# Kernel tuning notes

Measured on AMD Instinct MI355X. Metric: run time of the kernel, lower is better.

The kernel has to match this reference:

```python
import jax, jax.numpy as jnp
import numpy as np

B, C_IN, H, W = 1, 3, 96, 96
NB_CLASSES = 21
NB_ITER = 5
THETA_ALPHA, THETA_BETA, THETA_GAMMA = 160.0, 3.0, 3.0


def setup_inputs() -> dict:
    key = jax.random.key(0)
    ks = jax.random.split(key, 8)
    image = jax.random.uniform(ks[0], (B, C_IN, H, W), jnp.float32)
    net_w = jax.random.normal(ks[1], (NB_CLASSES, C_IN, 3, 3), jnp.float32) * 0.1
    net_b = jax.random.normal(ks[2], (NB_CLASSES,), jnp.float32) * 0.01
    sp_w = jax.random.normal(ks[3], (NB_CLASSES, NB_CLASSES), jnp.float32) * 0.1
    sp_b = jnp.zeros((NB_CLASSES,), jnp.float32)
    bl_w = jax.random.normal(ks[4], (NB_CLASSES, NB_CLASSES), jnp.float32) * 0.1
    bl_b = jnp.zeros((NB_CLASSES,), jnp.float32)
    comp_w = jax.random.normal(ks[5], (NB_CLASSES, NB_CLASSES), jnp.float32) * 0.1
    comp_b = jnp.zeros((NB_CLASSES,), jnp.float32)
    return {"image": image, "net_w": net_w, "net_b": net_b,
            "sp_w": sp_w, "sp_b": sp_b, "bl_w": bl_w, "bl_b": bl_b,
            "comp_w": comp_w, "comp_b": comp_b}


def _gauss_kernel(feat):
    # feat: [B, N, D] -> K[B, N, N] = exp(-||f_i - f_j||^2 / 2)
    sq = jnp.sum(feat * feat, axis=-1)
    d2 = sq[:, :, None] + sq[:, None, :] - 2.0 * jnp.einsum('bnd,bmd->bnm', feat, feat)
    return jnp.exp(-0.5 * jnp.maximum(d2, 0.0))


def _crf_forward(image, net_w, net_b, sp_w, sp_b, bl_w, bl_b, comp_w, comp_b):
    b, c_in, h, w = image.shape
    n = h * w
    nb_classes = net_w.shape[0]
    # unary network: 3x3 same conv
    unaries = jax.lax.conv_general_dilated(
        image, net_w, (1, 1), 'SAME',
        dimension_numbers=('NCHW', 'OIHW', 'NCHW')) + net_b[None, :, None, None]
    # feature-space Gaussian kernels (exact form the permutohedral lattice approximates)
    yy, xx = jnp.meshgrid(jnp.arange(h, dtype=jnp.float32),
                          jnp.arange(w, dtype=jnp.float32), indexing='ij')
    pos = jnp.stack([xx.ravel(), yy.ravel()], axis=-1)          # [N, 2]
    pos_b = jnp.broadcast_to(pos, (b, n, 2))
    img_flat = image.reshape(b, c_in, n).transpose(0, 2, 1)      # [B, N, Cin]
    k_sp = _gauss_kernel(pos_b / THETA_GAMMA)                    # spatial kernel
    k_bl = _gauss_kernel(jnp.concatenate(
        [pos_b / THETA_ALPHA, img_flat / THETA_BETA], axis=-1))  # bilateral kernel
    norm_sp = k_sp.sum(-1)                                       # [B, N]
    norm_bl = k_bl.sum(-1)

    def filt(k, norm, s):
        return jnp.einsum('bnm,bcm->bcn', k, s) / norm[:, None, :]

    u = unaries.reshape(b, nb_classes, n)
    q = u
    s = jax.nn.softmax(q, axis=1)
    for _ in range(NB_ITER):
        sp = filt(k_sp, norm_sp, s)
        bl = filt(k_bl, norm_bl, s)
        mp = (jnp.einsum('oc,bcn->bon', sp_w, sp) + sp_b[None, :, None]
              + jnp.einsum('oc,bcn->bon', bl_w, bl) + bl_b[None, :, None])
        pairwise = jnp.einsum('oc,bcn->bon', comp_w, mp) + comp_b[None, :, None]
        q = u - pairwise
        s = jax.nn.softmax(q, axis=1)
    return s.reshape(b, nb_classes, h, w)


def reference(image, net_w, net_b, sp_w, sp_b, bl_w, bl_b, comp_w, comp_b):
    return _crf_forward(image, net_w, net_b, sp_w, sp_b, bl_w, bl_b, comp_w, comp_b)
```

## Files before the change

### kernel.cpp

```cpp
#include <hip/hip_runtime.h>

#define NPIX 9216
#define IMH 96
#define IMW 96
#define NC 21
#define NCH 22
#define CP 24
#define NMON 126
#define RAD 15
#define NITER 5
#define MG 11
#define NMG 12
#define LDSS 260
#define MPAD 2816

__constant__ float GW[16] = {
    1.0f, 0.945959f, 0.800737f, 0.606531f, 0.411112f, 0.249352f,
    0.135335f, 0.0657285f, 0.0285655f, 0.0111090f, 0.00386592f,
    0.00120386f, 0.000335463f, 8.36523e-05f, 1.86640e-05f, 3.72665e-06f};

__constant__ float d_bk[5] = {1.000000f, 0.998959f, 0.509936f, 0.139441f, 0.070024f};

__global__ __launch_bounds__(64) void prep_kernel(
    const float* __restrict__ img, const float* __restrict__ net_w,
    const float* __restrict__ net_b,
    float* __restrict__ u_pm, float* __restrict__ s_pm, float* __restrict__ s_cm,
    float* __restrict__ phi, float* __restrict__ M0)
{
    __shared__ float wsh[567], bsh[21];
    __shared__ float sg_sh[NMON];
    const int tid = threadIdx.x;
    for (int i = tid; i < 567; i += 64) wsh[i] = net_w[i];
    if (tid < 21) bsh[tid] = net_b[tid];
    for (int m = tid; m < NMON; m += 64) {
        int e1 = 0, e2 = 0, e3 = 0, e4 = 0, e5 = 0, cnt = 0;
        bool done = false;
        for (int a = 0; a <= 4 && !done; a++)
            for (int b2 = 0; b2 <= 4 - a && !done; b2++)
                for (int c = 0; c <= 4 - a - b2 && !done; c++)
                    for (int d = 0; d <= 4 - a - b2 - c && !done; d++) {
                        const int rem = 4 - a - b2 - c - d;
                        if (m - cnt <= rem) {
                            e1 = a; e2 = b2; e3 = c; e4 = d; e5 = m - cnt; done = true;
                        } else cnt += rem + 1;
                    }
        const float fact[5] = {1.f, 1.f, 2.f, 6.f, 24.f};
        const int k = e1 + e2 + e3 + e4 + e5;
        sg_sh[m] = sqrtf(d_bk[k] * fact[k] /
                         (fact[e1] * fact[e2] * fact[e3] * fact[e4] * fact[e5]));
    }
    __syncthreads();

    const int px = blockIdx.x * 64 + tid;
    const int i = px / IMW, j = px % IMW;
    if (px < 2772) M0[px] = 0.f;

    float acc[NC];
    #pragma unroll
    for (int o = 0; o < NC; o++) acc[o] = bsh[o];
    for (int ci = 0; ci < 3; ci++)
        for (int ky = 0; ky < 3; ky++)
            for (int kx = 0; kx < 3; kx++) {
                const int ii = i + ky - 1, jj = j + kx - 1;
                float v = 0.f;
                if (ii >= 0 && ii < IMH && jj >= 0 && jj < IMW)
                    v = img[(ci * IMH + ii) * IMW + jj];
                #pragma unroll
                for (int o = 0; o < NC; o++)
                    acc[o] = fmaf(v, wsh[(ci * 3 + ky) * 3 + kx + o * 27], acc[o]);
            }
    {
        float4* up = (float4*)(u_pm + (size_t)px * CP);
        up[0] = make_float4(acc[0], acc[1], acc[2], acc[3]);
        up[1] = make_float4(acc[4], acc[5], acc[6], acc[7]);
        up[2] = make_float4(acc[8], acc[9], acc[10], acc[11]);
        up[3] = make_float4(acc[12], acc[13], acc[14], acc[15]);
        up[4] = make_float4(acc[16], acc[17], acc[18], acc[19]);
        up[5] = make_float4(acc[20], 0.f, 0.f, 0.f);
    }
    float mx = acc[0];
    #pragma unroll
    for (int o = 1; o < NC; o++) mx = fmaxf(mx, acc[o]);
    float sum = 0.f;
    #pragma unroll
    for (int o = 0; o < NC; o++) { acc[o] = __expf(acc[o] - mx); sum += acc[o]; }
    const float inv = 1.f / sum;
    #pragma unroll
    for (int o = 0; o < NC; o++) acc[o] *= inv;
    {
        float4* sp = (float4*)(s_pm + (size_t)px * CP);
        sp[0] = make_float4(acc[0], acc[1], acc[2], acc[3]);
        sp[1] = make_float4(acc[4], acc[5], acc[6], acc[7]);
        sp[2] = make_float4(acc[8], acc[9], acc[10], acc[11]);
        sp[3] = make_float4(acc[12], acc[13], acc[14], acc[15]);
        sp[4] = make_float4(acc[16], acc[17], acc[18], acc[19]);
        sp[5] = make_float4(acc[20], 1.f, 0.f, 0.f);
    }
    #pragma unroll
    for (int o = 0; o < NC; o++) s_cm[(size_t)o * NPIX + px] = acc[o];
    s_cm[(size_t)21 * NPIX + px] = 1.f;

    const float fv[5] = {(float)j * (1.0f / 160.0f), (float)i * (1.0f / 160.0f),
                         img[0 * NPIX + px] * (1.0f / 3.0f),
                         img[1 * NPIX + px] * (1.0f / 3.0f),
                         img[2 * NPIX + px] * (1.0f / 3.0f)};
    const float env = __expf(-0.5f * (fv[0]*fv[0] + fv[1]*fv[1] + fv[2]*fv[2] +
                                      fv[3]*fv[3] + fv[4]*fv[4]));
    {
        int m = 0;
        float p1 = env;
        #pragma unroll
        for (int e1 = 0; e1 <= 4; e1++) {
            float p2 = p1;
            #pragma unroll
            for (int e2 = 0; e2 <= 4 - e1; e2++) {
                float p3 = p2;
                #pragma unroll
                for (int e3 = 0; e3 <= 4 - e1 - e2; e3++) {
                    float p4 = p3;
                    #pragma unroll
                    for (int e4 = 0; e4 <= 4 - e1 - e2 - e3; e4++) {
                        float p5 = p4;
                        #pragma unroll
                        for (int e5 = 0; e5 <= 4 - e1 - e2 - e3 - e4; e5++) {
                            phi[(size_t)m * NPIX + px] = sg_sh[m] * p5;
                            ++m;
                            p5 *= fv[4];
                        }
                        p4 *= fv[3];
                    }
                    p3 *= fv[2];
                }
                p2 *= fv[1];
            }
            p1 *= fv[0];
        }
    }
}

__global__ __launch_bounds__(256) void k1_kernel(
    const float* __restrict__ s_pm, const float* __restrict__ s_cm,
    const float* __restrict__ phi, float* __restrict__ sx, float* __restrict__ M)
{
    __shared__ float smem[(NCH + MG) * LDSS];
    const int bid = blockIdx.x, tid = threadIdx.x;
    if (bid < NMG * 36) {
        const int g = bid / 36, chunk = bid % 36;
        const int m0 = g * MG;
        const int mcnt = (NMON - m0 < MG) ? (NMON - m0) : MG;
        float* s_sh = smem;
        float* p_sh = smem + NCH * LDSS;
        {
            const float4* sp = (const float4*)(s_pm + (size_t)(chunk * 256 + tid) * CP);
            #pragma unroll
            for (int v = 0; v < 6; v++) {
                const float4 t = sp[v];
                const int c = 4 * v;
                if (c < NCH)     s_sh[c * LDSS + tid] = t.x;
                if (c + 1 < NCH) s_sh[(c + 1) * LDSS + tid] = t.y;
                if (c + 2 < NCH) s_sh[(c + 2) * LDSS + tid] = t.z;
                if (c + 3 < NCH) s_sh[(c + 3) * LDSS + tid] = t.w;
            }
        }
        for (int idx = tid; idx < mcnt * 64; idx += 256) {
            const int mm = idx >> 6, p4 = idx & 63;
            const float4 t = *(const float4*)(phi + (size_t)(m0 + mm) * NPIX +
                                              chunk * 256 + p4 * 4);
            *(float4*)(p_sh + mm * LDSS + p4 * 4) = t;
        }
        __syncthreads();
        const int c = tid % NCH, msub = tid / NCH;
        if (msub < mcnt) {
            const float* sr = s_sh + c * LDSS;
            const float* pr = p_sh + msub * LDSS;
            float acc = 0.f;
            for (int p4 = 0; p4 < 64; p4++) {
                const float4 sv = *(const float4*)(sr + p4 * 4);
                const float4 pv = *(const float4*)(pr + p4 * 4);
                acc += pv.x * sv.x + pv.y * sv.y + pv.z * sv.z + pv.w * sv.w;
            }
            atomicAdd(&M[(m0 + msub) * NCH + c], acc);
        }
    } else {
        const int u2 = bid - NMG * 36;
        const int ch = u2 / 36, pc = u2 % 36;
        const int n = pc * 256 + tid, j = n % IMW;
        const float* row = s_cm + (size_t)ch * NPIX + (n - j);
        float a = GW[0] * row[j];
        #pragma unroll
        for (int d = 1; d <= RAD; d++) {
            const float l = (j - d >= 0) ? row[j - d] : 0.f;
            const float r = (j + d < IMW) ? row[j + d] : 0.f;
            a = fmaf(GW[d], l + r, a);
        }
        sx[(size_t)ch * NPIX + n] = a;
    }
}

__global__ __launch_bounds__(256) void k2_kernel(
    const float* __restrict__ sx, const float* __restrict__ phi,
    const float* __restrict__ M, float* __restrict__ Mnext,
    const float* __restrict__ u_pm,
    const float* __restrict__ sp_w, const float* __restrict__ sp_b,
    const float* __restrict__ bl_w, const float* __restrict__ bl_b,
    const float* __restrict__ comp_w, const float* __restrict__ comp_b,
    float* __restrict__ s_pm, float* __restrict__ s_cm,
    float* __restrict__ out, int write_out)
{
    __shared__ float Msh[NMON * CP];
    __shared__ float phi_sh[NMON * 32];
    __shared__ float cy_sh[32 * 25];
    __shared__ float blv_sh[32 * 25];
    __shared__ float mp_sh[32 * CP];
    __shared__ float q_sh[32 * CP];
    __shared__ float wsh[1386 + 63];
    const int tid = threadIdx.x;
    const int px0 = blockIdx.x * 32;
    const int i0 = px0 / IMW;

    for (int idx = tid; idx < NMON * CP; idx += 256) {
        const int mm = idx / CP, c = idx % CP;
        Msh[idx] = (c < NCH) ? M[mm * NCH + c] : 0.f;
    }
    for (int idx = tid; idx < 441; idx += 256) {
        wsh[idx] = sp_w[idx]; wsh[441 + idx] = bl_w[idx]; wsh[882 + idx] = comp_w[idx];
    }
    if (tid < 21) {
        wsh[1323 + tid] = sp_b[tid]; wsh[1344 + tid] = bl_b[tid];
        wsh[1365 + tid] = comp_b[tid];
    }
    if (blockIdx.x < 11) {
        const int idx = blockIdx.x * 256 + tid;
        if (idx < 2772) Mnext[idx] = 0.f;
    }
    for (int idx = tid; idx < NMON * 8; idx += 256) {
        const int m = idx >> 3, g = idx & 7;
        *(float4*)(phi_sh + m * 32 + g * 4) =
            *(const float4*)(phi + (size_t)m * NPIX + px0 + g * 4);
    }
    for (int task = tid; task < 24 * 32; task += 256) {
        const int ch = task >> 5, p = task & 31;
        if (ch < NCH) {
            const int n = px0 + p;
            const float* plane = sx + (size_t)ch * NPIX;
            float a = GW[0] * plane[n];
            #pragma unroll
            for (int d = 1; d <= RAD; d++) {
                const float t = (i0 - d >= 0) ? plane[n - d * IMW] : 0.f;
                const float b = (i0 + d < IMH) ? plane[n + d * IMW] : 0.f;
                a = fmaf(GW[d], t + b, a);
            }
            cy_sh[p * 25 + ch] = a;
        }
    }
    __syncthreads();

    {
        const int p = tid & 31, c0 = (tid >> 5) * 3;
        float a0 = 0.f, a1 = 0.f, a2 = 0.f;
        for (int mm = 0; mm < NMON; mm++) {
            const float ph = phi_sh[mm * 32 + p];
            const float* Mr = Msh + mm * CP + c0;
            a0 = fmaf(ph, Mr[0], a0);
            a1 = fmaf(ph, Mr[1], a1);
            a2 = fmaf(ph, Mr[2], a2);
        }
        if (c0 < NCH)     blv_sh[p * 25 + c0] = a0;
        if (c0 + 1 < NCH) blv_sh[p * 25 + c0 + 1] = a1;
        if (c0 + 2 < NCH) blv_sh[p * 25 + c0 + 2] = a2;
    }
    __syncthreads();

    for (int t = tid; t < 672; t += 256) {
        const int p = t & 31, o = t >> 5;
        const float* cyr = cy_sh + p * 25;
        const float* blr = blv_sh + p * 25;
        float dS = 0.f, dB = 0.f;
        #pragma unroll
        for (int c = 0; c < NC; c++) {
            dS = fmaf(wsh[o * NC + c], cyr[c], dS);
            dB = fmaf(wsh[441 + o * NC + c], blr[c], dB);
        }
        mp_sh[p * CP + o] = wsh[1323 + o] + wsh[1344 + o] +
                            dS / cyr[21] + dB / blr[21];
    }
    __syncthreads();

    for (int t = tid; t < 672; t += 256) {
        const int p = t & 31, o = t >> 5;
        const float* mpr = mp_sh + p * CP;
        float d = wsh[1365 + o];
        #pragma unroll
        for (int c = 0; c < NC; c++) d = fmaf(wsh[882 + o * NC + c], mpr[c], d);
        q_sh[p * CP + o] = u_pm[(size_t)(px0 + p) * CP + o] - d;
    }
    __syncthreads();

    if (tid < 32) {
        const int n = px0 + tid;
        float q[NC];
        #pragma unroll
        for (int o = 0; o < NC; o++) q[o] = q_sh[tid * CP + o];
        float mx = q[0];
        #pragma unroll
        for (int o = 1; o < NC; o++) mx = fmaxf(mx, q[o]);
        float sum = 0.f;
        #pragma unroll
        for (int o = 0; o < NC; o++) { q[o] = __expf(q[o] - mx); sum += q[o]; }
        const float inv = 1.f / sum;
        #pragma unroll
        for (int o = 0; o < NC; o++) q[o] *= inv;

        float4* sp = (float4*)(s_pm + (size_t)n * CP);
        sp[0] = make_float4(q[0], q[1], q[2], q[3]);
        sp[1] = make_float4(q[4], q[5], q[6], q[7]);
        sp[2] = make_float4(q[8], q[9], q[10], q[11]);
        sp[3] = make_float4(q[12], q[13], q[14], q[15]);
        sp[4] = make_float4(q[16], q[17], q[18], q[19]);
        sp[5] = make_float4(q[20], 1.f, 0.f, 0.f);
        #pragma unroll
        for (int o = 0; o < NC; o++) s_cm[(size_t)o * NPIX + n] = q[o];
        s_cm[(size_t)21 * NPIX + n] = 1.f;
        if (write_out)
            #pragma unroll
            for (int o = 0; o < NC; o++) out[(size_t)o * NPIX + n] = q[o];
    }
}

extern "C" void kernel_launch(void* const* d_in, const int* in_sizes, int n_in,
                              void* d_out, int out_size, void* d_ws, size_t ws_size,
                              hipStream_t stream) {
    const float* img    = (const float*)d_in[0];
    const float* net_w  = (const float*)d_in[1];
    const float* net_b  = (const float*)d_in[2];
    const float* sp_w   = (const float*)d_in[3];
    const float* sp_b   = (const float*)d_in[4];
    const float* bl_w   = (const float*)d_in[5];
    const float* bl_b   = (const float*)d_in[6];
    const float* comp_w = (const float*)d_in[7];
    const float* comp_b = (const float*)d_in[8];

    float* u_pm = (float*)d_ws;
    float* s_pm = u_pm + (size_t)NPIX * CP;
    float* s_cm = s_pm + (size_t)NPIX * CP;
    float* sx   = s_cm + (size_t)NCH * NPIX;
    float* phi  = sx + (size_t)NCH * NPIX;
    float* M    = phi + (size_t)NMON * NPIX;

    float* out = (float*)d_out;

    prep_kernel<<<dim3(144), dim3(64), 0, stream>>>(
        img, net_w, net_b, u_pm, s_pm, s_cm, phi, M);
    for (int it = 0; it < NITER; it++) {
        float* Mc = M + (it & 1) * MPAD;
        float* Mn = M + ((it + 1) & 1) * MPAD;
        k1_kernel<<<dim3(NMG * 36 + NCH * 36), dim3(256), 0, stream>>>(
            s_pm, s_cm, phi, sx, Mc);
        k2_kernel<<<dim3(288), dim3(256), 0, stream>>>(
            sx, phi, Mc, Mn, u_pm, sp_w, sp_b, bl_w, bl_b, comp_w, comp_b,
            s_pm, s_cm, out, it == NITER - 1 ? 1 : 0);
    }
}
```

Before: 218.5 us.

## Fuse all CRF stages into one persistent kernel with software grid barriers

Replaces the prep kernel and the ten per-iteration k1/k2 launches with a single persistent kernel of 256 blocks. The blocks loop over the former task grids and synchronise with an atomic-counter grid barrier plus sleep between stages, and shared memory is unioned across the stage roles. This removes the launch overhead and inter-kernel gaps of eleven small kernels. In exchange it adds barrier spin latency and an extra memset, and correctness depends on all 256 blocks being co-resident.

```diff
diff --git a/kernel.cpp b/kernel.cpp
--- a/kernel.cpp
+++ b/kernel.cpp
@@ -13,6 +13,9 @@
 #define NMG 12
 #define LDSS 260
 #define MPAD 2816
+#define NTASK1 (NMG * 36 + NCH * 36)
+#define NTASK2 288
+#define GRIDB 256
 
 __constant__ float GW[16] = {
     1.0f, 0.945959f, 0.800737f, 0.606531f, 0.411112f, 0.249352f,
@@ -21,309 +24,342 @@
 
 __constant__ float d_bk[5] = {1.000000f, 0.998959f, 0.509936f, 0.139441f, 0.070024f};
 
-__global__ __launch_bounds__(64) void prep_kernel(
+__device__ __forceinline__ void grid_bar(unsigned* cnt, unsigned& bidx) {
+    __syncthreads();
+    if (threadIdx.x == 0) {
+        __threadfence();
+        atomicAdd(cnt, 1u);
+        const unsigned target = GRIDB * (++bidx);
+        while (atomicAdd(cnt, 0u) < target)
+            __builtin_amdgcn_s_sleep(1);
+        __threadfence();
+    }
+    __syncthreads();
+}
+
+__global__ __launch_bounds__(256) void fused_kernel(
     const float* __restrict__ img, const float* __restrict__ net_w,
     const float* __restrict__ net_b,
-    float* __restrict__ u_pm, float* __restrict__ s_pm, float* __restrict__ s_cm,
-    float* __restrict__ phi, float* __restrict__ M0)
-{
-    __shared__ float wsh[567], bsh[21];
-    __shared__ float sg_sh[NMON];
-    const int tid = threadIdx.x;
-    for (int i = tid; i < 567; i += 64) wsh[i] = net_w[i];
-    if (tid < 21) bsh[tid] = net_b[tid];
-    for (int m = tid; m < NMON; m += 64) {
-        int e1 = 0, e2 = 0, e3 = 0, e4 = 0, e5 = 0, cnt = 0;
-        bool done = false;
-        for (int a = 0; a <= 4 && !done; a++)
-            for (int b2 = 0; b2 <= 4 - a && !done; b2++)
-                for (int c = 0; c <= 4 - a - b2 && !done; c++)
-                    for (int d = 0; d <= 4 - a - b2 - c && !done; d++) {
-                        const int rem = 4 - a - b2 - c - d;
-                        if (m - cnt <= rem) {
-                            e1 = a; e2 = b2; e3 = c; e4 = d; e5 = m - cnt; done = true;
-                        } else cnt += rem + 1;
-                    }
-        const float fact[5] = {1.f, 1.f, 2.f, 6.f, 24.f};
-        const int k = e1 + e2 + e3 + e4 + e5;
-        sg_sh[m] = sqrtf(d_bk[k] * fact[k] /
-                         (fact[e1] * fact[e2] * fact[e3] * fact[e4] * fact[e5]));
-    }
-    __syncthreads();
-
-    const int px = blockIdx.x * 64 + tid;
-    const int i = px / IMW, j = px % IMW;
-    if (px < 2772) M0[px] = 0.f;
-
-    float acc[NC];
-    #pragma unroll
-    for (int o = 0; o < NC; o++) acc[o] = bsh[o];
-    for (int ci = 0; ci < 3; ci++)
-        for (int ky = 0; ky < 3; ky++)
-            for (int kx = 0; kx < 3; kx++) {
-                const int ii = i + ky - 1, jj = j + kx - 1;
-                float v = 0.f;
-                if (ii >= 0 && ii < IMH && jj >= 0 && jj < IMW)
-                    v = img[(ci * IMH + ii) * IMW + jj];
-                #pragma unroll
-                for (int o = 0; o < NC; o++)
-                    acc[o] = fmaf(v, wsh[(ci * 3 + ky) * 3 + kx + o * 27], acc[o]);
-            }
-    {
-        float4* up = (float4*)(u_pm + (size_t)px * CP);
-        up[0] = make_float4(acc[0], acc[1], acc[2], acc[3]);
-        up[1] = make_float4(acc[4], acc[5], acc[6], acc[7]);
-        up[2] = make_float4(acc[8], acc[9], acc[10], acc[11]);
-        up[3] = make_float4(acc[12], acc[13], acc[14], acc[15]);
-        up[4] = make_float4(acc[16], acc[17], acc[18], acc[19]);
-        up[5] = make_float4(acc[20], 0.f, 0.f, 0.f);
-    }
-    float mx = acc[0];
-    #pragma unroll
-    for (int o = 1; o < NC; o++) mx = fmaxf(mx, acc[o]);
-    float sum = 0.f;
-    #pragma unroll
-    for (int o = 0; o < NC; o++) { acc[o] = __expf(acc[o] - mx); sum += acc[o]; }
-    const float inv = 1.f / sum;
-    #pragma unroll
-    for (int o = 0; o < NC; o++) acc[o] *= inv;
-    {
-        float4* sp = (float4*)(s_pm + (size_t)px * CP);
-        sp[0] = make_float4(acc[0], acc[1], acc[2], acc[3]);
-        sp[1] = make_float4(acc[4], acc[5], acc[6], acc[7]);
-        sp[2] = make_float4(acc[8], acc[9], acc[10], acc[11]);
-        sp[3] = make_float4(acc[12], acc[13], acc[14], acc[15]);
-        sp[4] = make_float4(acc[16], acc[17], acc[18], acc[19]);
-        sp[5] = make_float4(acc[20], 1.f, 0.f, 0.f);
-    }
-    #pragma unroll
-    for (int o = 0; o < NC; o++) s_cm[(size_t)o * NPIX + px] = acc[o];
-    s_cm[(size_t)21 * NPIX + px] = 1.f;
-
-    const float fv[5] = {(float)j * (1.0f / 160.0f), (float)i * (1.0f / 160.0f),
-                         img[0 * NPIX + px] * (1.0f / 3.0f),
-                         img[1 * NPIX + px] * (1.0f / 3.0f),
-                         img[2 * NPIX + px] * (1.0f / 3.0f)};
-    const float env = __expf(-0.5f * (fv[0]*fv[0] + fv[1]*fv[1] + fv[2]*fv[2] +
-                                      fv[3]*fv[3] + fv[4]*fv[4]));
-    {
-        int m = 0;
-        float p1 = env;
-        #pragma unroll
-        for (int e1 = 0; e1 <= 4; e1++) {
-            float p2 = p1;
-            #pragma unroll
-            for (int e2 = 0; e2 <= 4 - e1; e2++) {
-                float p3 = p2;
-                #pragma unroll
-                for (int e3 = 0; e3 <= 4 - e1 - e2; e3++) {
-                    float p4 = p3;
-                    #pragma unroll
-                    for (int e4 = 0; e4 <= 4 - e1 - e2 - e3; e4++) {
-                        float p5 = p4;
-                        #pragma unroll
-                        for (int e5 = 0; e5 <= 4 - e1 - e2 - e3 - e4; e5++) {
-                            phi[(size_t)m * NPIX + px] = sg_sh[m] * p5;
-                            ++m;
-                            p5 *= fv[4];
-                        }
-                        p4 *= fv[3];
-                    }
-                    p3 *= fv[2];
-                }
-                p2 *= fv[1];
-            }
-            p1 *= fv[0];
-        }
-    }
-}
-
-__global__ __launch_bounds__(256) void k1_kernel(
-    const float* __restrict__ s_pm, const float* __restrict__ s_cm,
-    const float* __restrict__ phi, float* __restrict__ sx, float* __restrict__ M)
-{
-    __shared__ float smem[(NCH + MG) * LDSS];
-    const int bid = blockIdx.x, tid = threadIdx.x;
-    if (bid < NMG * 36) {
-        const int g = bid / 36, chunk = bid % 36;
-        const int m0 = g * MG;
-        const int mcnt = (NMON - m0 < MG) ? (NMON - m0) : MG;
-        float* s_sh = smem;
-        float* p_sh = smem + NCH * LDSS;
-        {
-            const float4* sp = (const float4*)(s_pm + (size_t)(chunk * 256 + tid) * CP);
-            #pragma unroll
-            for (int v = 0; v < 6; v++) {
-                const float4 t = sp[v];
-                const int c = 4 * v;
-                if (c < NCH)     s_sh[c * LDSS + tid] = t.x;
-                if (c + 1 < NCH) s_sh[(c + 1) * LDSS + tid] = t.y;
-                if (c + 2 < NCH) s_sh[(c + 2) * LDSS + tid] = t.z;
-                if (c + 3 < NCH) s_sh[(c + 3) * LDSS + tid] = t.w;
-            }
-        }
-        for (int idx = tid; idx < mcnt * 64; idx += 256) {
-            const int mm = idx >> 6, p4 = idx & 63;
-            const float4 t = *(const float4*)(phi + (size_t)(m0 + mm) * NPIX +
-                                              chunk * 256 + p4 * 4);
-            *(float4*)(p_sh + mm * LDSS + p4 * 4) = t;
-        }
-        __syncthreads();
-        const int c = tid % NCH, msub = tid / NCH;
-        if (msub < mcnt) {
-            const float* sr = s_sh + c * LDSS;
-            const float* pr = p_sh + msub * LDSS;
-            float acc = 0.f;
-            for (int p4 = 0; p4 < 64; p4++) {
-                const float4 sv = *(const float4*)(sr + p4 * 4);
-                const float4 pv = *(const float4*)(pr + p4 * 4);
-                acc += pv.x * sv.x + pv.y * sv.y + pv.z * sv.z + pv.w * sv.w;
-            }
-            atomicAdd(&M[(m0 + msub) * NCH + c], acc);
-        }
-    } else {
-        const int u2 = bid - NMG * 36;
-        const int ch = u2 / 36, pc = u2 % 36;
-        const int n = pc * 256 + tid, j = n % IMW;
-        const float* row = s_cm + (size_t)ch * NPIX + (n - j);
-        float a = GW[0] * row[j];
-        #pragma unroll
-        for (int d = 1; d <= RAD; d++) {
-            const float l = (j - d >= 0) ? row[j - d] : 0.f;
-            const float r = (j + d < IMW) ? row[j + d] : 0.f;
-            a = fmaf(GW[d], l + r, a);
-        }
-        sx[(size_t)ch * NPIX + n] = a;
-    }
-}
-
-__global__ __launch_bounds__(256) void k2_kernel(
-    const float* __restrict__ sx, const float* __restrict__ phi,
-    const float* __restrict__ M, float* __restrict__ Mnext,
-    const float* __restrict__ u_pm,
     const float* __restrict__ sp_w, const float* __restrict__ sp_b,
     const float* __restrict__ bl_w, const float* __restrict__ bl_b,
     const float* __restrict__ comp_w, const float* __restrict__ comp_b,
-    float* __restrict__ s_pm, float* __restrict__ s_cm,
-    float* __restrict__ out, int write_out)
+    float* __restrict__ u_pm, float* __restrict__ s_pm, float* __restrict__ s_cm,
+    float* __restrict__ sx, float* __restrict__ phi, float* __restrict__ M,
+    unsigned* __restrict__ barcnt, float* __restrict__ out)
 {
-    __shared__ float Msh[NMON * CP];
-    __shared__ float phi_sh[NMON * 32];
-    __shared__ float cy_sh[32 * 25];
-    __shared__ float blv_sh[32 * 25];
-    __shared__ float mp_sh[32 * CP];
-    __shared__ float q_sh[32 * CP];
-    __shared__ float wsh[1386 + 63];
+    __shared__ union {
+        float a_smem[(NCH + MG) * LDSS];
+        struct {
+            float Msh[NMON * CP];
+            float phi_sh[NMON * 32];
+            float cy_sh[32 * 25];
+            float blv_sh[32 * 25];
+            float mp_sh[32 * CP];
+            float q_sh[32 * CP];
+            float wsh[1386 + 63];
+        } b;
+        struct {
+            float wsh[567];
+            float bsh[21];
+            float sg[NMON];
+        } p;
+    } sh;
+
     const int tid = threadIdx.x;
-    const int px0 = blockIdx.x * 32;
-    const int i0 = px0 / IMW;
-
-    for (int idx = tid; idx < NMON * CP; idx += 256) {
-        const int mm = idx / CP, c = idx % CP;
-        Msh[idx] = (c < NCH) ? M[mm * NCH + c] : 0.f;
+    const int bid = blockIdx.x;
+    unsigned bidx = 0;
+
+    if (bid < 36) {
+        for (int i2 = tid; i2 < 567; i2 += 256) sh.p.wsh[i2] = net_w[i2];
+        if (tid < 21) sh.p.bsh[tid] = net_b[tid];
+        for (int m = tid; m < NMON; m += 256) {
+            int e1 = 0, e2 = 0, e3 = 0, e4 = 0, e5 = 0, cnt = 0;
+            bool done = false;
+            for (int a = 0; a <= 4 && !done; a++)
+                for (int b2 = 0; b2 <= 4 - a && !done; b2++)
+                    for (int c = 0; c <= 4 - a - b2 && !done; c++)
+                        for (int d = 0; d <= 4 - a - b2 - c && !done; d++) {
+                            const int rem = 4 - a - b2 - c - d;
+                            if (m - cnt <= rem) {
+                                e1 = a; e2 = b2; e3 = c; e4 = d; e5 = m - cnt;
+                                done = true;
+                            } else cnt += rem + 1;
+                        }
+            const float fact[5] = {1.f, 1.f, 2.f, 6.f, 24.f};
+            const int k = e1 + e2 + e3 + e4 + e5;
+            sh.p.sg[m] = sqrtf(d_bk[k] * fact[k] /
+                               (fact[e1] * fact[e2] * fact[e3] * fact[e4] * fact[e5]));
+        }
+        __syncthreads();
+
+        const int px = bid * 256 + tid;
+        const int i = px / IMW, j = px % IMW;
+        if (px < 2772) M[px] = 0.f;
+
+        float acc[NC];
+        #pragma unroll
+        for (int o = 0; o < NC; o++) acc[o] = sh.p.bsh[o];
+        for (int ci = 0; ci < 3; ci++)
+            for (int ky = 0; ky < 3; ky++)
+                for (int kx = 0; kx < 3; kx++) {
+                    const int ii = i + ky - 1, jj = j + kx - 1;
+                    float v = 0.f;
+                    if (ii >= 0 && ii < IMH && jj >= 0 && jj < IMW)
+                        v = img[(ci * IMH + ii) * IMW + jj];
+                    #pragma unroll
+                    for (int o = 0; o < NC; o++)
+                        acc[o] = fmaf(v, sh.p.wsh[(ci * 3 + ky) * 3 + kx + o * 27],
+                                      acc[o]);
+                }
+        {
+            float4* up = (float4*)(u_pm + (size_t)px * CP);
+            up[0] = make_float4(acc[0], acc[1], acc[2], acc[3]);
+            up[1] = make_float4(acc[4], acc[5], acc[6], acc[7]);
+            up[2] = make_float4(acc[8], acc[9], acc[10], acc[11]);
+            up[3] = make_float4(acc[12], acc[13], acc[14], acc[15]);
+            up[4] = make_float4(acc[16], acc[17], acc[18], acc[19]);
+            up[5] = make_float4(acc[20], 0.f, 0.f, 0.f);
+        }
+        float mx = acc[0];
+        #pragma unroll
+        for (int o = 1; o < NC; o++) mx = fmaxf(mx, acc[o]);
+        float sum = 0.f;
+        #pragma unroll
+        for (int o = 0; o < NC; o++) { acc[o] = __expf(acc[o] - mx); sum += acc[o]; }
+        const float inv = 1.f / sum;
+        #pragma unroll
+        for (int o = 0; o < NC; o++) acc[o] *= inv;
+        {
+            float4* sp = (float4*)(s_pm + (size_t)px * CP);
+            sp[0] = make_float4(acc[0], acc[1], acc[2], acc[3]);
+            sp[1] = make_float4(acc[4], acc[5], acc[6], acc[7]);
+            sp[2] = make_float4(acc[8], acc[9], acc[10], acc[11]);
+            sp[3] = make_float4(acc[12], acc[13], acc[14], acc[15]);
+            sp[4] = make_float4(acc[16], acc[17], acc[18], acc[19]);
+            sp[5] = make_float4(acc[20], 1.f, 0.f, 0.f);
+        }
+        #pragma unroll
+        for (int o = 0; o < NC; o++) s_cm[(size_t)o * NPIX + px] = acc[o];
+        s_cm[(size_t)21 * NPIX + px] = 1.f;
+
+        const float fv[5] = {(float)j * (1.0f / 160.0f), (float)i * (1.0f / 160.0f),
+                             img[0 * NPIX + px] * (1.0f / 3.0f),
+                             img[1 * NPIX + px] * (1.0f / 3.0f),
+                             img[2 * NPIX + px] * (1.0f / 3.0f)};
+        const float env = __expf(-0.5f * (fv[0]*fv[0] + fv[1]*fv[1] + fv[2]*fv[2] +
+                                          fv[3]*fv[3] + fv[4]*fv[4]));
+        {
+            int m = 0;
+            float p1 = env;
+            #pragma unroll
+            for (int e1 = 0; e1 <= 4; e1++) {
+                float p2 = p1;
+                #pragma unroll
+                for (int e2 = 0; e2 <= 4 - e1; e2++) {
+                    float p3 = p2;
+                    #pragma unroll
+                    for (int e3 = 0; e3 <= 4 - e1 - e2; e3++) {
+                        float p4 = p3;
+                        #pragma unroll
+                        for (int e4 = 0; e4 <= 4 - e1 - e2 - e3; e4++) {
+                            float p5 = p4;
+                            #pragma unroll
+                            for (int e5 = 0; e5 <= 4 - e1 - e2 - e3 - e4; e5++) {
+                                phi[(size_t)m * NPIX + px] = sh.p.sg[m] * p5;
+                                ++m;
+                                p5 *= fv[4];
+                            }
+                            p4 *= fv[3];
+                        }
+                        p3 *= fv[2];
+                    }
+                    p2 *= fv[1];
+                }
+                p1 *= fv[0];
+            }
+        }
     }
-    for (int idx = tid; idx < 441; idx += 256) {
-        wsh[idx] = sp_w[idx]; wsh[441 + idx] = bl_w[idx]; wsh[882 + idx] = comp_w[idx];
-    }
-    if (tid < 21) {
-        wsh[1323 + tid] = sp_b[tid]; wsh[1344 + tid] = bl_b[tid];
-        wsh[1365 + tid] = comp_b[tid];
-    }
-    if (blockIdx.x < 11) {
-        const int idx = blockIdx.x * 256 + tid;
-        if (idx < 2772) Mnext[idx] = 0.f;
-    }
-    for (int idx = tid; idx < NMON * 8; idx += 256) {
-        const int m = idx >> 3, g = idx & 7;
-        *(float4*)(phi_sh + m * 32 + g * 4) =
-            *(const float4*)(phi + (size_t)m * NPIX + px0 + g * 4);
-    }
-    for (int task = tid; task < 24 * 32; task += 256) {
-        const int ch = task >> 5, p = task & 31;
-        if (ch < NCH) {
-            const int n = px0 + p;
-            const float* plane = sx + (size_t)ch * NPIX;
-            float a = GW[0] * plane[n];
-            #pragma unroll
-            for (int d = 1; d <= RAD; d++) {
-                const float t = (i0 - d >= 0) ? plane[n - d * IMW] : 0.f;
-                const float b = (i0 + d < IMH) ? plane[n + d * IMW] : 0.f;
-                a = fmaf(GW[d], t + b, a);
-            }
-            cy_sh[p * 25 + ch] = a;
-        }
-    }
-    __syncthreads();
-
-    {
-        const int p = tid & 31, c0 = (tid >> 5) * 3;
-        float a0 = 0.f, a1 = 0.f, a2 = 0.f;
-        for (int mm = 0; mm < NMON; mm++) {
-            const float ph = phi_sh[mm * 32 + p];
-            const float* Mr = Msh + mm * CP + c0;
-            a0 = fmaf(ph, Mr[0], a0);
-            a1 = fmaf(ph, Mr[1], a1);
-            a2 = fmaf(ph, Mr[2], a2);
-        }
-        if (c0 < NCH)     blv_sh[p * 25 + c0] = a0;
-        if (c0 + 1 < NCH) blv_sh[p * 25 + c0 + 1] = a1;
-        if (c0 + 2 < NCH) blv_sh[p * 25 + c0 + 2] = a2;
-    }
-    __syncthreads();
-
-    for (int t = tid; t < 672; t += 256) {
-        const int p = t & 31, o = t >> 5;
-        const float* cyr = cy_sh + p * 25;
-        const float* blr = blv_sh + p * 25;
-        float dS = 0.f, dB = 0.f;
-        #pragma unroll
-        for (int c = 0; c < NC; c++) {
-            dS = fmaf(wsh[o * NC + c], cyr[c], dS);
-            dB = fmaf(wsh[441 + o * NC + c], blr[c], dB);
-        }
-        mp_sh[p * CP + o] = wsh[1323 + o] + wsh[1344 + o] +
-                            dS / cyr[21] + dB / blr[21];
-    }
-    __syncthreads();
-
-    for (int t = tid; t < 672; t += 256) {
-        const int p = t & 31, o = t >> 5;
-        const float* mpr = mp_sh + p * CP;
-        float d = wsh[1365 + o];
-        #pragma unroll
-        for (int c = 0; c < NC; c++) d = fmaf(wsh[882 + o * NC + c], mpr[c], d);
-        q_sh[p * CP + o] = u_pm[(size_t)(px0 + p) * CP + o] - d;
-    }
-    __syncthreads();
-
-    if (tid < 32) {
-        const int n = px0 + tid;
-        float q[NC];
-        #pragma unroll
-        for (int o = 0; o < NC; o++) q[o] = q_sh[tid * CP + o];
-        float mx = q[0];
-        #pragma unroll
-        for (int o = 1; o < NC; o++) mx = fmaxf(mx, q[o]);
-        float sum = 0.f;
-        #pragma unroll
-        for (int o = 0; o < NC; o++) { q[o] = __expf(q[o] - mx); sum += q[o]; }
-        const float inv = 1.f / sum;
-        #pragma unroll
-        for (int o = 0; o < NC; o++) q[o] *= inv;
-
-        float4* sp = (float4*)(s_pm + (size_t)n * CP);
-        sp[0] = make_float4(q[0], q[1], q[2], q[3]);
-        sp[1] = make_float4(q[4], q[5], q[6], q[7]);
-        sp[2] = make_float4(q[8], q[9], q[10], q[11]);
-        sp[3] = make_float4(q[12], q[13], q[14], q[15]);
-        sp[4] = make_float4(q[16], q[17], q[18], q[19]);
-        sp[5] = make_float4(q[20], 1.f, 0.f, 0.f);
-        #pragma unroll
-        for (int o = 0; o < NC; o++) s_cm[(size_t)o * NPIX + n] = q[o];
-        s_cm[(size_t)21 * NPIX + n] = 1.f;
-        if (write_out)
-            #pragma unroll
-            for (int o = 0; o < NC; o++) out[(size_t)o * NPIX + n] = q[o];
+    grid_bar(barcnt, bidx);
+
+    for (int it = 0; it < NITER; it++) {
+        float* Mc = M + (it & 1) * MPAD;
+        float* Mn = M + ((it + 1) & 1) * MPAD;
+
+        for (int t = bid; t < NTASK1; t += GRIDB) {
+            __syncthreads();
+            if (t < NMG * 36) {
+                const int g = t / 36, chunk = t % 36;
+                const int m0 = g * MG;
+                const int mcnt = (NMON - m0 < MG) ? (NMON - m0) : MG;
+                float* s_sh = sh.a_smem;
+                float* p_sh = sh.a_smem + NCH * LDSS;
+                {
+                    const float4* sp =
+                        (const float4*)(s_pm + (size_t)(chunk * 256 + tid) * CP);
+                    #pragma unroll
+                    for (int v = 0; v < 6; v++) {
+                        const float4 tv = sp[v];
+                        const int c = 4 * v;
+                        if (c < NCH)     s_sh[c * LDSS + tid] = tv.x;
+                        if (c + 1 < NCH) s_sh[(c + 1) * LDSS + tid] = tv.y;
+                        if (c + 2 < NCH) s_sh[(c + 2) * LDSS + tid] = tv.z;
+                        if (c + 3 < NCH) s_sh[(c + 3) * LDSS + tid] = tv.w;
+                    }
+                }
+                for (int idx = tid; idx < mcnt * 64; idx += 256) {
+                    const int mm = idx >> 6, p4 = idx & 63;
+                    const float4 tv = *(const float4*)(phi + (size_t)(m0 + mm) * NPIX +
+                                                       chunk * 256 + p4 * 4);
+                    *(float4*)(p_sh + mm * LDSS + p4 * 4) = tv;
+                }
+                __syncthreads();
+                const int c = tid % NCH, msub = tid / NCH;
+                if (msub < mcnt) {
+                    const float* sr = s_sh + c * LDSS;
+                    const float* pr = p_sh + msub * LDSS;
+                    float acc = 0.f;
+                    for (int p4 = 0; p4 < 64; p4++) {
+                        const float4 sv = *(const float4*)(sr + p4 * 4);
+                        const float4 pv = *(const float4*)(pr + p4 * 4);
+                        acc += pv.x * sv.x + pv.y * sv.y + pv.z * sv.z + pv.w * sv.w;
+                    }
+                    atomicAdd(&Mc[(m0 + msub) * NCH + c], acc);
+                }
+            } else {
+                const int u2 = t - NMG * 36;
+                const int ch = u2 / 36, pc = u2 % 36;
+                const int n = pc * 256 + tid, j = n % IMW;
+                const float* row = s_cm + (size_t)ch * NPIX + (n - j);
+                float a = GW[0] * row[j];
+                #pragma unroll
+                for (int d = 1; d <= RAD; d++) {
+                    const float l = (j - d >= 0) ? row[j - d] : 0.f;
+                    const float r = (j + d < IMW) ? row[j + d] : 0.f;
+                    a = fmaf(GW[d], l + r, a);
+                }
+                sx[(size_t)ch * NPIX + n] = a;
+            }
+        }
+        grid_bar(barcnt, bidx);
+
+        for (int t = bid; t < NTASK2; t += GRIDB) {
+            __syncthreads();
+            const int px0 = t * 32;
+            const int i0 = px0 / IMW;
+
+            for (int idx = tid; idx < NMON * CP; idx += 256) {
+                const int mm = idx / CP, c = idx % CP;
+                sh.b.Msh[idx] = (c < NCH) ? Mc[mm * NCH + c] : 0.f;
+            }
+            for (int idx = tid; idx < 441; idx += 256) {
+                sh.b.wsh[idx] = sp_w[idx];
+                sh.b.wsh[441 + idx] = bl_w[idx];
+                sh.b.wsh[882 + idx] = comp_w[idx];
+            }
+            if (tid < 21) {
+                sh.b.wsh[1323 + tid] = sp_b[tid];
+                sh.b.wsh[1344 + tid] = bl_b[tid];
+                sh.b.wsh[1365 + tid] = comp_b[tid];
+            }
+            if (t < 11) {
+                const int idx = t * 256 + tid;
+                if (idx < 2772) Mn[idx] = 0.f;
+            }
+            for (int idx = tid; idx < NMON * 8; idx += 256) {
+                const int m = idx >> 3, g = idx & 7;
+                *(float4*)(sh.b.phi_sh + m * 32 + g * 4) =
+                    *(const float4*)(phi + (size_t)m * NPIX + px0 + g * 4);
+            }
+            for (int task = tid; task < 24 * 32; task += 256) {
+                const int ch = task >> 5, p = task & 31;
+                if (ch < NCH) {
+                    const int n = px0 + p;
+                    const float* plane = sx + (size_t)ch * NPIX;
+                    float a = GW[0] * plane[n];
+                    #pragma unroll
+                    for (int d = 1; d <= RAD; d++) {
+                        const float tt = (i0 - d >= 0) ? plane[n - d * IMW] : 0.f;
+                        const float bb = (i0 + d < IMH) ? plane[n + d * IMW] : 0.f;
+                        a = fmaf(GW[d], tt + bb, a);
+                    }
+                    sh.b.cy_sh[p * 25 + ch] = a;
+                }
+            }
+            __syncthreads();
+
+            {
+                const int p = tid & 31, c0 = (tid >> 5) * 3;
+                float a0 = 0.f, a1 = 0.f, a2 = 0.f;
+                for (int mm = 0; mm < NMON; mm++) {
+                    const float ph = sh.b.phi_sh[mm * 32 + p];
+                    const float* Mr = sh.b.Msh + mm * CP + c0;
+                    a0 = fmaf(ph, Mr[0], a0);
+                    a1 = fmaf(ph, Mr[1], a1);
+                    a2 = fmaf(ph, Mr[2], a2);
+                }
+                if (c0 < NCH)     sh.b.blv_sh[p * 25 + c0] = a0;
+                if (c0 + 1 < NCH) sh.b.blv_sh[p * 25 + c0 + 1] = a1;
+                if (c0 + 2 < NCH) sh.b.blv_sh[p * 25 + c0 + 2] = a2;
+            }
+            __syncthreads();
+
+            for (int t2 = tid; t2 < 672; t2 += 256) {
+                const int p = t2 & 31, o = t2 >> 5;
+                const float* cyr = sh.b.cy_sh + p * 25;
+                const float* blr = sh.b.blv_sh + p * 25;
+                float dS = 0.f, dB = 0.f;
+                #pragma unroll
+                for (int c = 0; c < NC; c++) {
+                    dS = fmaf(sh.b.wsh[o * NC + c], cyr[c], dS);
+                    dB = fmaf(sh.b.wsh[441 + o * NC + c], blr[c], dB);
+                }
+                sh.b.mp_sh[p * CP + o] = sh.b.wsh[1323 + o] + sh.b.wsh[1344 + o] +
+                                         dS / cyr[21] + dB / blr[21];
+            }
+            __syncthreads();
+
+            for (int t2 = tid; t2 < 672; t2 += 256) {
+                const int p = t2 & 31, o = t2 >> 5;
+                const float* mpr = sh.b.mp_sh + p * CP;
+                float d = sh.b.wsh[1365 + o];
+                #pragma unroll
+                for (int c = 0; c < NC; c++)
+                    d = fmaf(sh.b.wsh[882 + o * NC + c], mpr[c], d);
+                sh.b.q_sh[p * CP + o] = u_pm[(size_t)(px0 + p) * CP + o] - d;
+            }
+            __syncthreads();
+
+            if (tid < 32) {
+                const int n = px0 + tid;
+                float q[NC];
+                #pragma unroll
+                for (int o = 0; o < NC; o++) q[o] = sh.b.q_sh[tid * CP + o];
+                float mx = q[0];
+                #pragma unroll
+                for (int o = 1; o < NC; o++) mx = fmaxf(mx, q[o]);
+                float sum = 0.f;
+                #pragma unroll
+                for (int o = 0; o < NC; o++) { q[o] = __expf(q[o] - mx); sum += q[o]; }
+                const float inv = 1.f / sum;
+                #pragma unroll
+                for (int o = 0; o < NC; o++) q[o] *= inv;
+
+                float4* sp = (float4*)(s_pm + (size_t)n * CP);
+                sp[0] = make_float4(q[0], q[1], q[2], q[3]);
+                sp[1] = make_float4(q[4], q[5], q[6], q[7]);
+                sp[2] = make_float4(q[8], q[9], q[10], q[11]);
+                sp[3] = make_float4(q[12], q[13], q[14], q[15]);
+                sp[4] = make_float4(q[16], q[17], q[18], q[19]);
+                sp[5] = make_float4(q[20], 1.f, 0.f, 0.f);
+                #pragma unroll
+                for (int o = 0; o < NC; o++) s_cm[(size_t)o * NPIX + n] = q[o];
+                s_cm[(size_t)21 * NPIX + n] = 1.f;
+                if (it == NITER - 1)
+                    #pragma unroll
+                    for (int o = 0; o < NC; o++) out[(size_t)o * NPIX + n] = q[o];
+            }
+        }
+        if (it != NITER - 1) grid_bar(barcnt, bidx);
     }
 }
 
@@ -346,18 +382,13 @@
     float* sx   = s_cm + (size_t)NCH * NPIX;
     float* phi  = sx + (size_t)NCH * NPIX;
     float* M    = phi + (size_t)NMON * NPIX;
+    unsigned* barcnt = (unsigned*)(M + 2 * MPAD);
 
     float* out = (float*)d_out;
 
-    prep_kernel<<<dim3(144), dim3(64), 0, stream>>>(
-        img, net_w, net_b, u_pm, s_pm, s_cm, phi, M);
-    for (int it = 0; it < NITER; it++) {
-        float* Mc = M + (it & 1) * MPAD;
-        float* Mn = M + ((it + 1) & 1) * MPAD;
-        k1_kernel<<<dim3(NMG * 36 + NCH * 36), dim3(256), 0, stream>>>(
-            s_pm, s_cm, phi, sx, Mc);
-        k2_kernel<<<dim3(288), dim3(256), 0, stream>>>(
-            sx, phi, Mc, Mn, u_pm, sp_w, sp_b, bl_w, bl_b, comp_w, comp_b,
-            s_pm, s_cm, out, it == NITER - 1 ? 1 : 0);
-    }
+    hipMemsetAsync(barcnt, 0, 8, stream);
+
+    fused_kernel<<<dim3(GRIDB), dim3(256), 0, stream>>>(
+        img, net_w, net_b, sp_w, sp_b, bl_w, bl_b, comp_w, comp_b,
+        u_pm, s_pm, s_cm, sx, phi, M, barcnt, out);
 }
```

Result: slower. 489.0 us (+123.9%).
